# Kernel tuning notes

Hardware: AMD Instinct MI355X
Metric: run time of the kernel (lower is better)

The kernel has to match this reference:

```python
import jax, jax.numpy as jnp
import numpy as np


def setup_inputs() -> dict:
    key = jax.random.key(0)
    # logits in [0,1): safe for the unstabilized exp used by the source module
    data = jax.random.uniform(key, (2048, 32000), dtype=jnp.float32)
    return {"data": data}


def reference(data):
    # Faithful to source: e**x / sum(e**x) along the normalization axis,
    # with NO max-subtraction (the original does plain math.e ** x).
    e = jnp.exp(data)                          # [B, V]
    return e / jnp.sum(e, axis=-1, keepdims=True)
```

## Files before the change

kernel.cpp:

```cpp
#include <hip/hip_runtime.h>


#define SM_THREADS 1024
#define SM_V 32000
#define SM_FULL 7
#define SM_REM 832
#define SM_ROWS_PER_BLOCK 8

typedef float f32x4 __attribute__((ext_vector_type(4)));

__global__ __launch_bounds__(SM_THREADS, 1)
void softmax_rowwise_kernel(const float* __restrict__ in,
                            float* __restrict__ out) {
    const int tid = threadIdx.x;
    const int wave = tid >> 6;
    const int lane = tid & 63;

    __shared__ float wsum[2][SM_THREADS / 64];

    const int row0 = blockIdx.x * SM_ROWS_PER_BLOCK;

    for (int r = 0; r < SM_ROWS_PER_BLOCK; ++r) {
        const size_t base = (size_t)(row0 + r) * SM_V;
        const f32x4* __restrict__ inrow  = reinterpret_cast<const f32x4*>(in + base);
        f32x4* __restrict__       outrow = reinterpret_cast<f32x4*>(out + base);

        f32x4 e[8];
        float lsum = 0.0f;

        #pragma unroll
        for (int k = 0; k < SM_FULL; ++k) {
            f32x4 x = __builtin_nontemporal_load(&inrow[tid + k * SM_THREADS]);
            f32x4 ev;
            ev.x = __expf(x.x);
            ev.y = __expf(x.y);
            ev.z = __expf(x.z);
            ev.w = __expf(x.w);
            e[k] = ev;
            lsum += (ev.x + ev.y) + (ev.z + ev.w);
        }
        if (tid < SM_REM) {
            f32x4 x = __builtin_nontemporal_load(&inrow[tid + SM_FULL * SM_THREADS]);
            f32x4 ev;
            ev.x = __expf(x.x);
            ev.y = __expf(x.y);
            ev.z = __expf(x.z);
            ev.w = __expf(x.w);
            e[7] = ev;
            lsum += (ev.x + ev.y) + (ev.z + ev.w);
        }

        #pragma unroll
        for (int off = 32; off > 0; off >>= 1)
            lsum += __shfl_down(lsum, off, 64);

        if (lane == 0) wsum[r & 1][wave] = lsum;
        __syncthreads();

        float total = 0.0f;
        #pragma unroll
        for (int i = 0; i < SM_THREADS / 64; ++i)
            total += wsum[r & 1][i];

        const float inv = 1.0f / total;

        #pragma unroll
        for (int k = 0; k < SM_FULL; ++k) {
            f32x4 ev = e[k];
            f32x4 o;
            o.x = ev.x * inv;
            o.y = ev.y * inv;
            o.z = ev.z * inv;
            o.w = ev.w * inv;
            __builtin_nontemporal_store(o, &outrow[tid + k * SM_THREADS]);
        }
        if (tid < SM_REM) {
            f32x4 ev = e[7];
            f32x4 o;
            o.x = ev.x * inv;
            o.y = ev.y * inv;
            o.z = ev.z * inv;
            o.w = ev.w * inv;
            __builtin_nontemporal_store(o, &outrow[tid + SM_FULL * SM_THREADS]);
        }
    }
}

extern "C" void kernel_launch(void* const* d_in, const int* in_sizes, int n_in,
                              void* d_out, int out_size, void* d_ws, size_t ws_size,
                              hipStream_t stream) {
    (void)n_in; (void)d_ws; (void)ws_size; (void)out_size;
    const float* in = (const float*)d_in[0];
    float* out = (float*)d_out;
    const int rows = in_sizes[0] / SM_V;
    const int blocks = rows / SM_ROWS_PER_BLOCK;
    softmax_rowwise_kernel<<<dim3(blocks), dim3(SM_THREADS), 0, stream>>>(in, out);
}
```

Measured before the change: 98.96 us.

## Prefetch next row while storing current row in softmax kernel

Software-pipelines the per-block row loop. The loads for row r+1 are issued before the normalized stores of row r, so read latency overlaps the write traffic and the reduction barrier. This doubles the register footprint for row data (x and e arrays, 64 floats each per thread), which is still within budget at one 1024-thread block per CU. The double-buffered shared sums keep the barrier use safe.

```diff
diff --git a/kernel.cpp b/kernel.cpp
--- a/kernel.cpp
+++ b/kernel.cpp
@@ -5,9 +5,65 @@
 #define SM_V 32000
 #define SM_FULL 7
 #define SM_REM 832
-#define SM_ROWS_PER_BLOCK 8
+#define SM_RPB 8
 
 typedef float f32x4 __attribute__((ext_vector_type(4)));
+
+__device__ __forceinline__ void load_row(const float* __restrict__ in,
+                                         size_t base, int tid, f32x4 x[8]) {
+    const f32x4* __restrict__ inrow = reinterpret_cast<const f32x4*>(in + base);
+    #pragma unroll
+    for (int k = 0; k < SM_FULL; ++k)
+        x[k] = __builtin_nontemporal_load(&inrow[tid + k * SM_THREADS]);
+    if (tid < SM_REM)
+        x[7] = __builtin_nontemporal_load(&inrow[tid + SM_FULL * SM_THREADS]);
+}
+
+__device__ __forceinline__ float exp_row(const f32x4 x[8], f32x4 e[8], int tid) {
+    float lsum = 0.0f;
+    #pragma unroll
+    for (int k = 0; k < SM_FULL; ++k) {
+        f32x4 ev;
+        ev.x = __expf(x[k].x);
+        ev.y = __expf(x[k].y);
+        ev.z = __expf(x[k].z);
+        ev.w = __expf(x[k].w);
+        e[k] = ev;
+        lsum += (ev.x + ev.y) + (ev.z + ev.w);
+    }
+    if (tid < SM_REM) {
+        f32x4 ev;
+        ev.x = __expf(x[7].x);
+        ev.y = __expf(x[7].y);
+        ev.z = __expf(x[7].z);
+        ev.w = __expf(x[7].w);
+        e[7] = ev;
+        lsum += (ev.x + ev.y) + (ev.z + ev.w);
+    }
+    return lsum;
+}
+
+__device__ __forceinline__ void store_row(float* __restrict__ out, size_t base,
+                                          int tid, const f32x4 e[8], float inv) {
+    f32x4* __restrict__ outrow = reinterpret_cast<f32x4*>(out + base);
+    #pragma unroll
+    for (int k = 0; k < SM_FULL; ++k) {
+        f32x4 o;
+        o.x = e[k].x * inv;
+        o.y = e[k].y * inv;
+        o.z = e[k].z * inv;
+        o.w = e[k].w * inv;
+        __builtin_nontemporal_store(o, &outrow[tid + k * SM_THREADS]);
+    }
+    if (tid < SM_REM) {
+        f32x4 o;
+        o.x = e[7].x * inv;
+        o.y = e[7].y * inv;
+        o.z = e[7].z * inv;
+        o.w = e[7].w * inv;
+        __builtin_nontemporal_store(o, &outrow[tid + SM_FULL * SM_THREADS]);
+    }
+}
 
 __global__ __launch_bounds__(SM_THREADS, 1)
 void softmax_rowwise_kernel(const float* __restrict__ in,
@@ -18,70 +74,46 @@
 
     __shared__ float wsum[2][SM_THREADS / 64];
 
-    const int row0 = blockIdx.x * SM_ROWS_PER_BLOCK;
+    const int row0 = blockIdx.x * SM_RPB;
 
-    for (int r = 0; r < SM_ROWS_PER_BLOCK; ++r) {
-        const size_t base = (size_t)(row0 + r) * SM_V;
-        const f32x4* __restrict__ inrow  = reinterpret_cast<const f32x4*>(in + base);
-        f32x4* __restrict__       outrow = reinterpret_cast<f32x4*>(out + base);
+    f32x4 x[8], e[8];
 
-        f32x4 e[8];
-        float lsum = 0.0f;
+    load_row(in, (size_t)row0 * SM_V, tid, x);
+    float lsum = exp_row(x, e, tid);
 
-        #pragma unroll
-        for (int k = 0; k < SM_FULL; ++k) {
-            f32x4 x = __builtin_nontemporal_load(&inrow[tid + k * SM_THREADS]);
-            f32x4 ev;
-            ev.x = __expf(x.x);
-            ev.y = __expf(x.y);
-            ev.z = __expf(x.z);
-            ev.w = __expf(x.w);
-            e[k] = ev;
-            lsum += (ev.x + ev.y) + (ev.z + ev.w);
-        }
-        if (tid < SM_REM) {
-            f32x4 x = __builtin_nontemporal_load(&inrow[tid + SM_FULL * SM_THREADS]);
-            f32x4 ev;
-            ev.x = __expf(x.x);
-            ev.y = __expf(x.y);
-            ev.z = __expf(x.z);
-            ev.w = __expf(x.w);
-            e[7] = ev;
-            lsum += (ev.x + ev.y) + (ev.z + ev.w);
-        }
+    #pragma unroll
+    for (int off = 32; off > 0; off >>= 1)
+        lsum += __shfl_down(lsum, off, 64);
+    if (lane == 0) wsum[0][wave] = lsum;
+    __syncthreads();
+    float total = 0.0f;
+    #pragma unroll
+    for (int i = 0; i < SM_THREADS / 64; ++i)
+        total += wsum[0][i];
+    float inv = 1.0f / total;
 
-        #pragma unroll
-        for (int off = 32; off > 0; off >>= 1)
-            lsum += __shfl_down(lsum, off, 64);
+    for (int r = 0; r < SM_RPB; ++r) {
+        f32x4 xn[8];
+        const bool more = (r + 1 < SM_RPB);
 
-        if (lane == 0) wsum[r & 1][wave] = lsum;
-        __syncthreads();
+        if (more)
+            load_row(in, (size_t)(row0 + r + 1) * SM_V, tid, xn);
 
-        float total = 0.0f;
-        #pragma unroll
-        for (int i = 0; i < SM_THREADS / 64; ++i)
-            total += wsum[r & 1][i];
+        store_row(out, (size_t)(row0 + r) * SM_V, tid, e, inv);
 
-        const float inv = 1.0f / total;
-
-        #pragma unroll
-        for (int k = 0; k < SM_FULL; ++k) {
-            f32x4 ev = e[k];
-            f32x4 o;
-            o.x = ev.x * inv;
-            o.y = ev.y * inv;
-            o.z = ev.z * inv;
-            o.w = ev.w * inv;
-            __builtin_nontemporal_store(o, &outrow[tid + k * SM_THREADS]);
-        }
-        if (tid < SM_REM) {
-            f32x4 ev = e[7];
-            f32x4 o;
-            o.x = ev.x * inv;
-            o.y = ev.y * inv;
-            o.z = ev.z * inv;
-            o.w = ev.w * inv;
-            __builtin_nontemporal_store(o, &outrow[tid + SM_FULL * SM_THREADS]);
+        if (more) {
+            lsum = exp_row(xn, e, tid);
+            #pragma unroll
+            for (int off = 32; off > 0; off >>= 1)
+                lsum += __shfl_down(lsum, off, 64);
+            const int p = (r + 1) & 1;
+            if (lane == 0) wsum[p][wave] = lsum;
+            __syncthreads();
+            total = 0.0f;
+            #pragma unroll
+            for (int i = 0; i < SM_THREADS / 64; ++i)
+                total += wsum[p][i];
+            inv = 1.0f / total;
         }
     }
 }
@@ -93,6 +125,6 @@
     const float* in = (const float*)d_in[0];
     float* out = (float*)d_out;
     const int rows = in_sizes[0] / SM_V;
-    const int blocks = rows / SM_ROWS_PER_BLOCK;
+    const int blocks = rows / SM_RPB;
     softmax_rowwise_kernel<<<dim3(blocks), dim3(SM_THREADS), 0, stream>>>(in, out);
 }
```

After: 93.99 us. 1.05x faster.
